# Kernel tuning notes

Measured on AMD Instinct MI355X. Metric: run time of the kernel, lower is better.

Reference implementation:

```python
import jax, jax.numpy as jnp
import numpy as np

FACTOR = 2  # upsample factor per spatial dim


def setup_inputs() -> dict:
    key = jax.random.key(0)
    k1, k2, k3 = jax.random.split(key, 3)
    B, C_in, C_out, H, W_ = 8, 128, 128, 64, 64
    x = jax.random.normal(k1, (B, C_in, H, W_), dtype=jnp.float32)
    # conv3x3 params (OIHW), fan-in scaled init like torch Conv2d default scale
    fan_in = C_in * 3 * 3
    W = jax.random.normal(k2, (C_out, C_in, 3, 3), dtype=jnp.float32) / np.sqrt(fan_in)
    b = jax.random.normal(k3, (C_out,), dtype=jnp.float32) * 0.01
    return {"x": x, "W": W, "b": b}


def reference(x, W, b):
    h = jnp.repeat(jnp.repeat(x, FACTOR, axis=2), FACTOR, axis=3)  # [B,C,2H,2W]
    # conv3x3: stride 1, padding 1
    out = jax.lax.conv_general_dilated(
        h, W,
        window_strides=(1, 1),
        padding=((1, 1), (1, 1)),
        dimension_numbers=("NCHW", "OIHW", "NCHW"),
    )
    return out + b[None, :, None, None]
```

## Files before the change

### kernel.cpp

```cpp
#include <hip/hip_runtime.h>
#include <stdint.h>

typedef short bf16x8 __attribute__((ext_vector_type(8)));
typedef float f32x4 __attribute__((ext_vector_type(4)));
typedef float f32x16 __attribute__((ext_vector_type(16)));

#define NCI 128
#define NCO 128
#define HIN 64
#define HP  66
#define NB  8

__device__ __forceinline__ unsigned short f32_to_bf16(float f) {
    union { float f; uint32_t u; } v; v.f = f;
    return (unsigned short)((v.u + 0x7FFFu + ((v.u >> 16) & 1u)) >> 16);
}

__device__ __forceinline__ void gl_lds16(const void* g, void* l) {
    __builtin_amdgcn_global_load_lds(
        (const __attribute__((address_space(1))) unsigned int*)g,
        (__attribute__((address_space(3))) unsigned int*)l, 16, 0, 0);
}

__device__ __forceinline__ float weff_sum(const float* wp, int py, int px, int ty, int tx) {
    float s = 0.f;
    #pragma unroll
    for (int ky = 0; ky < 3; ++ky) {
        bool iy = (py == 0) ? (ty == 0 ? (ky == 0) : (ky >= 1))
                            : (ty == 0 ? (ky <= 1) : (ky == 2));
        if (!iy) continue;
        #pragma unroll
        for (int kx = 0; kx < 3; ++kx) {
            bool ix = (px == 0) ? (tx == 0 ? (kx == 0) : (kx >= 1))
                                : (tx == 0 ? (kx <= 1) : (kx == 2));
            if (ix) s += wp[ky * 3 + kx];
        }
    }
    return s;
}

__global__ __launch_bounds__(256) void prep_kernel(
        const float* __restrict__ W, const float* __restrict__ x,
        unsigned short* __restrict__ Aw8, unsigned short* __restrict__ xq) {
    if (blockIdx.x < 1024) {
        int idx = blockIdx.x * 256 + threadIdx.x;
        int e   = idx & 7;
        int l   = (idx >> 3) & 63;
        int fm  = (idx >> 9) & 1;
        int s   = (idx >> 10) & 31;
        int coh = (idx >> 15) & 1;
        int par = idx >> 16;
        int co = coh * 64 + fm * 32 + (l & 31);
        int k  = s * 16 + (l >> 5) * 8 + e;
        int tap = k >> 7, ci = k & 127;
        Aw8[idx] = f32_to_bf16(weff_sum(W + (co * NCI + ci) * 9,
                                        par >> 1, par & 1, tap >> 1, tap & 1));
    } else {
        const int bb = blockIdx.x - 1024;
        const int b = bb / HP, hp = bb % HP;
        const int t = threadIdx.x;
        if (hp == 0 || hp == HP - 1) {
            bf16x8 z = (bf16x8){0, 0, 0, 0, 0, 0, 0, 0};
            for (int i = t; i < 4 * HP * 4; i += 256) {
                int g = i / (HP * 4), rem = i % (HP * 4);
                unsigned short* dst = xq +
                    ((((size_t)(b * 4 + g) * HP + hp) * HP) << 5) + rem * 8;
                *(bf16x8*)dst = z;
            }
            return;
        }
        const int h = hp - 1;
        if (t < 32) {
            bf16x8 z = (bf16x8){0, 0, 0, 0, 0, 0, 0, 0};
            int g = t >> 3, wpc = ((t >> 2) & 1) * (HP - 1), q = t & 3;
            unsigned short* dst = xq +
                ((((size_t)(b * 4 + g) * HP + hp) * HP + wpc) << 5) + q * 8;
            *(bf16x8*)dst = z;
        }
        const int w = t & 63, g = t >> 6;
        const float* src = x + ((size_t)(b * NCI + g * 32) * (HIN * HIN)) + h * HIN + w;
        unsigned short* dst = xq +
            ((((size_t)(b * 4 + g) * HP + hp) * HP + (w + 1)) << 5);
        #pragma unroll
        for (int q = 0; q < 4; ++q) {
            bf16x8 v;
            #pragma unroll
            for (int j = 0; j < 8; ++j)
                v[j] = (short)f32_to_bf16(src[(size_t)(q * 8 + j) * (HIN * HIN)]);
            *(bf16x8*)(dst + q * 8) = v;
        }
    }
}

__global__ __launch_bounds__(512, 2) void upconv16_kernel(
        const unsigned short* __restrict__ xq, const unsigned short* __restrict__ Aw8,
        const float* __restrict__ bv, float* __restrict__ out) {
    __shared__ __align__(16) unsigned short A_lds[32768];
    __shared__ __align__(16) unsigned short B_lds[42240];
    const int d = blockIdx.x;
    const int bi  = d & 7;
    const int py  = (d >> 3) & 1;
    const int px  = (d >> 4) & 1;
    const int coh = (d >> 5) & 1;
    const int ys  = d >> 6;
    const int tid = threadIdx.x, lane = tid & 63, wv = tid >> 6;
    const int sph = wv & 1, ol = wv >> 1;
    const int l31 = lane & 31, lh = lane >> 5;
    const int par = py * 2 + px;

    const unsigned short* Ag = Aw8 + (((size_t)(par * 2 + coh)) << 15);
    #pragma unroll
    for (int i = 0; i < 8; ++i) {
        const int u = i * 512 + tid;
        gl_lds16(Ag + u * 8, &A_lds[u * 8]);
    }
    #pragma unroll
    for (int i = 0; i < 11; ++i) {
        const int u = i * 512 + tid;
        if (u < 5280) {
            const int qs = u & 15, cell = u >> 4;
            const int r = cell / 66, c = cell - r * 66;
            const int q = qs ^ (c & 15);
            const int hp = ys * 4 + py + r;
            const unsigned short* gb = xq +
                ((((size_t)(bi * 4 + (q >> 2)) * HP + hp) * HP + c) << 5) + (q & 3) * 8;
            gl_lds16(gb, &B_lds[u * 8]);
        }
    }
    asm volatile("s_waitcnt vmcnt(0)" ::: "memory");
    __builtin_amdgcn_s_barrier();

    f32x16 acc[2];
    #pragma unroll
    for (int i = 0; i < 2; ++i)
        #pragma unroll
        for (int q = 0; q < 16; ++q)
            acc[i][q] = 0.f;

    #pragma unroll
    for (int s = 0; s < 32; ++s) {
        const int ty = s >> 4, tx = (s >> 3) & 1;
        const int q = (s & 7) * 2 + lh;
        const int r = ol + ty;
        const int c = sph * 32 + l31 + px + tx;
        const int qs = q ^ (c & 15);
        const bf16x8 bfr = *(const bf16x8*)&B_lds[(((r * 66 + c) << 4) + qs) * 8];
        const unsigned short* ap = &A_lds[(s << 10) + lane * 8];
        __builtin_amdgcn_s_setprio(1);
        acc[0] = __builtin_amdgcn_mfma_f32_32x32x16_bf16(
            *(const bf16x8*)ap, bfr, acc[0], 0, 0, 0);
        acc[1] = __builtin_amdgcn_mfma_f32_32x32x16_bf16(
            *(const bf16x8*)(ap + 512), bfr, acc[1], 0, 0, 0);
        __builtin_amdgcn_s_setprio(0);
    }

    const int yy = 2 * (ys * 4 + ol) + py;
    const int xx = 2 * (sph * 32 + l31) + px;
    #pragma unroll
    for (int fm = 0; fm < 2; ++fm) {
        #pragma unroll
        for (int j = 0; j < 16; ++j) {
            const int row = (j & 3) + 8 * (j >> 2) + 4 * lh;
            const int co = coh * 64 + fm * 32 + row;
            out[(((size_t)(bi * NCO + co)) << 14) + yy * 128 + xx] = acc[fm][j] + bv[co];
        }
    }
}

__global__ void weff_flat_kernel(const float* __restrict__ W,
                                 unsigned short* __restrict__ Aw) {
    int idx = blockIdx.x * 256 + threadIdx.x;
    int par = idx >> 16;
    int co  = (idx >> 9) & 127;
    int k   = idx & 511;
    int tap = k >> 7, ci = k & 127;
    Aw[idx] = f32_to_bf16(weff_sum(W + (co * NCI + ci) * 9,
                                   par >> 1, par & 1, tap >> 1, tap & 1));
}

__global__ __launch_bounds__(256) void upconv_fb_kernel(
        const float* __restrict__ x, const unsigned short* __restrict__ Aw,
        const float* __restrict__ bv, float* __restrict__ out) {
    __shared__ __align__(16) unsigned short A_lds[128 * 32];
    __shared__ __align__(16) unsigned short B_lds[128 * 32];
    const int par = blockIdx.y, py = par >> 1, px = par & 1;
    const int s0 = blockIdx.x * 128;
    const int bimg = s0 >> 12;
    const int oy0 = (s0 >> 6) & 63;
    const int tid = threadIdx.x;
    const int lane = tid & 63, wave = tid >> 6;
    const int wm = wave >> 1, wn = wave & 1;
    const float* xb = x + bimg * (NCI * HIN * HIN);
    f32x4 acc[4][4];
    #pragma unroll
    for (int i = 0; i < 4; ++i)
        #pragma unroll
        for (int j = 0; j < 4; ++j)
            acc[i][j] = (f32x4){0.f, 0.f, 0.f, 0.f};
    for (int kt = 0; kt < 16; ++kt) {
        const int tap = kt >> 2, ci0 = (kt & 3) * 32;
        const int ty = tap >> 1, tx = tap & 1;
        #pragma unroll
        for (int i = 0; i < 2; ++i) {
            int c = i * 256 + tid;
            *(bf16x8*)(&A_lds[c * 8]) = *(const bf16x8*)(Aw +
                ((par * 128 + (c >> 2)) * 512 + kt * 32 + (c & 3) * 8));
        }
        #pragma unroll
        for (int i = 0; i < 2; ++i) {
            int tsk = i * 256 + tid;
            int n = tsk & 127, kg = tsk >> 7;
            int r = n >> 6, ox = n & 63;
            int row = oy0 + r - 1 + py + ty;
            int col = ox - 1 + px + tx;
            bool ok = (row >= 0) & (row < HIN) & (col >= 0) & (col < HIN);
            const float* xp = xb + (((ci0 + kg * 8) * HIN + row) * HIN + col);
            bf16x8 v;
            #pragma unroll
            for (int q = 0; q < 8; ++q) {
                float f = ok ? xp[q * (HIN * HIN)] : 0.f;
                v[q] = (short)f32_to_bf16(f);
            }
            *(bf16x8*)(&B_lds[n * 32 + kg * 8]) = v;
        }
        __syncthreads();
        const int seg = (lane >> 4) * 8, rl2 = lane & 15;
        bf16x8 af[4], bfr[4];
        #pragma unroll
        for (int f = 0; f < 4; ++f)
            af[f] = *(const bf16x8*)(&A_lds[(wm * 64 + f * 16 + rl2) * 32 + seg]);
        #pragma unroll
        for (int f = 0; f < 4; ++f)
            bfr[f] = *(const bf16x8*)(&B_lds[(wn * 64 + f * 16 + rl2) * 32 + seg]);
        #pragma unroll
        for (int fm = 0; fm < 4; ++fm)
            #pragma unroll
            for (int fn = 0; fn < 4; ++fn)
                acc[fm][fn] = __builtin_amdgcn_mfma_f32_16x16x32_bf16(
                    af[fm], bfr[fn], acc[fm][fn], 0, 0, 0);
        __syncthreads();
    }
    #pragma unroll
    for (int fm = 0; fm < 4; ++fm) {
        const int co_b = wm * 64 + fm * 16 + (lane >> 4) * 4;
        float bias4[4];
        #pragma unroll
        for (int j = 0; j < 4; ++j) bias4[j] = bv[co_b + j];
        #pragma unroll
        for (int fn = 0; fn < 4; ++fn) {
            int n = wn * 64 + fn * 16 + (lane & 15);
            int s = s0 + n;
            int ox = s & 63, oy = (s >> 6) & 63, bi2 = s >> 12;
            int yy = 2 * oy + py, xx = 2 * ox + px;
            float* op = out + ((size_t)bi2 * 128 * 128 * 128) + (size_t)yy * 128 + xx;
            #pragma unroll
            for (int j = 0; j < 4; ++j)
                op[(size_t)(co_b + j) * (128 * 128)] = acc[fm][fn][j] + bias4[j];
        }
    }
}

extern "C" void kernel_launch(void* const* d_in, const int* in_sizes, int n_in,
                              void* d_out, int out_size, void* d_ws, size_t ws_size,
                              hipStream_t stream) {
    const float* x  = (const float*)d_in[0];
    const float* W  = (const float*)d_in[1];
    const float* bv = (const float*)d_in[2];
    float* out = (float*)d_out;
    unsigned short* Aw = (unsigned short*)d_ws;
    const size_t aw_bytes = (size_t)4 * 2 * 32 * 2 * 512 * sizeof(unsigned short);
    const size_t xq_bytes = (size_t)NB * 4 * HP * HP * 32 * sizeof(unsigned short);

    if (ws_size >= aw_bytes + xq_bytes) {
        unsigned short* xq = (unsigned short*)((char*)d_ws + aw_bytes);
        prep_kernel<<<1024 + NB * HP, 256, 0, stream>>>(W, x, Aw, xq);
        upconv16_kernel<<<1024, 512, 0, stream>>>(xq, Aw, bv, out);
    } else {
        weff_flat_kernel<<<1024, 256, 0, stream>>>(W, Aw);
        upconv_fb_kernel<<<dim3(256, 4), 256, 0, stream>>>(x, Aw, bv, out);
    }
}
```

Measured before the change: 41.40 us.

## Stream weights from global into registers, drop column padding, widen per-wave tile

The conv kernel now uses 256 threads, and each wave computes a 64x64 output tile (2x2 MFMA fragments) in place of a 64x32 one. Weight fragments are no longer staged in LDS; they are read straight from global memory into a triple-buffered register ring, prefetched three steps ahead. The padded-column layout of the quantized input is removed, and out-of-range columns are zeroed by a per-lane select, which shrinks LDS use and the prep work. This lowers LDS footprint and improves B-fragment reuse, at the cost of more registers, global-latency exposure on the weight loads, and extra select logic.

```diff
diff --git a/kernel.cpp b/kernel.cpp
--- a/kernel.cpp
+++ b/kernel.cpp
@@ -8,7 +8,6 @@
 #define NCI 128
 #define NCO 128
 #define HIN 64
-#define HP  66
 #define NB  8
 
 __device__ __forceinline__ unsigned short f32_to_bf16(float f) {
@@ -41,7 +40,7 @@
 
 __global__ __launch_bounds__(256) void prep_kernel(
         const float* __restrict__ W, const float* __restrict__ x,
-        unsigned short* __restrict__ Aw8, unsigned short* __restrict__ xq) {
+        unsigned short* __restrict__ Aw9, unsigned short* __restrict__ xq) {
     if (blockIdx.x < 1024) {
         int idx = blockIdx.x * 256 + threadIdx.x;
         int e   = idx & 7;
@@ -53,34 +52,26 @@
         int co = coh * 64 + fm * 32 + (l & 31);
         int k  = s * 16 + (l >> 5) * 8 + e;
         int tap = k >> 7, ci = k & 127;
-        Aw8[idx] = f32_to_bf16(weff_sum(W + (co * NCI + ci) * 9,
+        Aw9[idx] = f32_to_bf16(weff_sum(W + (co * NCI + ci) * 9,
                                         par >> 1, par & 1, tap >> 1, tap & 1));
     } else {
         const int bb = blockIdx.x - 1024;
-        const int b = bb / HP, hp = bb % HP;
+        const int b = bb / 66, hp = bb % 66;
         const int t = threadIdx.x;
-        if (hp == 0 || hp == HP - 1) {
+        unsigned short* rowp = xq + ((((size_t)b * 4) * 66 + hp) * 64) * 32;
+        if (hp == 0 || hp == 65) {
             bf16x8 z = (bf16x8){0, 0, 0, 0, 0, 0, 0, 0};
-            for (int i = t; i < 4 * HP * 4; i += 256) {
-                int g = i / (HP * 4), rem = i % (HP * 4);
-                unsigned short* dst = xq +
-                    ((((size_t)(b * 4 + g) * HP + hp) * HP) << 5) + rem * 8;
-                *(bf16x8*)dst = z;
+            for (int i = t; i < 1024; i += 256) {
+                int g = i >> 8, rem = i & 255;
+                int w = rem >> 2, q = rem & 3;
+                *(bf16x8*)(xq + (((((size_t)(b * 4 + g)) * 66 + hp) * 64 + w) << 5) + q * 8) = z;
             }
             return;
         }
         const int h = hp - 1;
-        if (t < 32) {
-            bf16x8 z = (bf16x8){0, 0, 0, 0, 0, 0, 0, 0};
-            int g = t >> 3, wpc = ((t >> 2) & 1) * (HP - 1), q = t & 3;
-            unsigned short* dst = xq +
-                ((((size_t)(b * 4 + g) * HP + hp) * HP + wpc) << 5) + q * 8;
-            *(bf16x8*)dst = z;
-        }
         const int w = t & 63, g = t >> 6;
         const float* src = x + ((size_t)(b * NCI + g * 32) * (HIN * HIN)) + h * HIN + w;
-        unsigned short* dst = xq +
-            ((((size_t)(b * 4 + g) * HP + hp) * HP + (w + 1)) << 5);
+        unsigned short* dst = xq + (((((size_t)(b * 4 + g)) * 66 + hp) * 64 + w) << 5);
         #pragma unroll
         for (int q = 0; q < 4; ++q) {
             bf16x8 v;
@@ -92,77 +83,91 @@
     }
 }
 
-__global__ __launch_bounds__(512, 2) void upconv16_kernel(
-        const unsigned short* __restrict__ xq, const unsigned short* __restrict__ Aw8,
+__global__ __launch_bounds__(256, 2) void upconv17_kernel(
+        const unsigned short* __restrict__ xq, const unsigned short* __restrict__ Aw9,
         const float* __restrict__ bv, float* __restrict__ out) {
-    __shared__ __align__(16) unsigned short A_lds[32768];
-    __shared__ __align__(16) unsigned short B_lds[42240];
+    __shared__ __align__(16) unsigned short B_lds[40960];
     const int d = blockIdx.x;
     const int bi  = d & 7;
     const int py  = (d >> 3) & 1;
     const int px  = (d >> 4) & 1;
     const int coh = (d >> 5) & 1;
     const int ys  = d >> 6;
-    const int tid = threadIdx.x, lane = tid & 63, wv = tid >> 6;
-    const int sph = wv & 1, ol = wv >> 1;
+    const int tid = threadIdx.x, lane = tid & 63, ol = tid >> 6;
     const int l31 = lane & 31, lh = lane >> 5;
     const int par = py * 2 + px;
 
-    const unsigned short* Ag = Aw8 + (((size_t)(par * 2 + coh)) << 15);
-    #pragma unroll
-    for (int i = 0; i < 8; ++i) {
-        const int u = i * 512 + tid;
-        gl_lds16(Ag + u * 8, &A_lds[u * 8]);
-    }
-    #pragma unroll
-    for (int i = 0; i < 11; ++i) {
-        const int u = i * 512 + tid;
-        if (u < 5280) {
-            const int qs = u & 15, cell = u >> 4;
-            const int r = cell / 66, c = cell - r * 66;
-            const int q = qs ^ (c & 15);
-            const int hp = ys * 4 + py + r;
-            const unsigned short* gb = xq +
-                ((((size_t)(bi * 4 + (q >> 2)) * HP + hp) * HP + c) << 5) + (q & 3) * 8;
-            gl_lds16(gb, &B_lds[u * 8]);
-        }
-    }
+    #pragma unroll
+    for (int i = 0; i < 20; ++i) {
+        const int u = i * 256 + tid;
+        const int qs = u & 15, cell = u >> 4;
+        const int r = cell >> 6, w = cell & 63;
+        const int q = qs ^ (w & 15);
+        const int hp = ys * 4 + py + r;
+        const unsigned short* gb = xq +
+            (((((size_t)(bi * 4 + (q >> 2))) * 66 + hp) * 64 + w) << 5) + (q & 3) * 8;
+        gl_lds16(gb, &B_lds[u * 8]);
+    }
+
+    const unsigned short* Ag = Aw9 + (((size_t)(par * 2 + coh)) << 15);
+    bf16x8 Abuf[3][2];
+    auto loadA = [&](bf16x8* Ad, int s) {
+        const unsigned short* p = Ag + (s << 10) + lane * 8;
+        Ad[0] = *(const bf16x8*)p;
+        Ad[1] = *(const bf16x8*)(p + 512);
+    };
+    loadA(Abuf[0], 0);
+    loadA(Abuf[1], 1);
+    loadA(Abuf[2], 2);
     asm volatile("s_waitcnt vmcnt(0)" ::: "memory");
     __builtin_amdgcn_s_barrier();
 
-    f32x16 acc[2];
+    f32x16 acc[2][2];
     #pragma unroll
     for (int i = 0; i < 2; ++i)
         #pragma unroll
-        for (int q = 0; q < 16; ++q)
-            acc[i][q] = 0.f;
+        for (int j = 0; j < 2; ++j)
+            #pragma unroll
+            for (int q = 0; q < 16; ++q)
+                acc[i][j][q] = 0.f;
 
     #pragma unroll
     for (int s = 0; s < 32; ++s) {
+        bf16x8* Ac = Abuf[s % 3];
         const int ty = s >> 4, tx = (s >> 3) & 1;
         const int q = (s & 7) * 2 + lh;
         const int r = ol + ty;
-        const int c = sph * 32 + l31 + px + tx;
-        const int qs = q ^ (c & 15);
-        const bf16x8 bfr = *(const bf16x8*)&B_lds[(((r * 66 + c) << 4) + qs) * 8];
-        const unsigned short* ap = &A_lds[(s << 10) + lane * 8];
         __builtin_amdgcn_s_setprio(1);
-        acc[0] = __builtin_amdgcn_mfma_f32_32x32x16_bf16(
-            *(const bf16x8*)ap, bfr, acc[0], 0, 0, 0);
-        acc[1] = __builtin_amdgcn_mfma_f32_32x32x16_bf16(
-            *(const bf16x8*)(ap + 512), bfr, acc[1], 0, 0, 0);
+        #pragma unroll
+        for (int fn = 0; fn < 2; ++fn) {
+            const int wr = fn * 32 + l31 + px + tx - 1;
+            const bool valid = (unsigned)wr < 64u;
+            const int w = valid ? wr : 0;
+            const int qs = q ^ (w & 15);
+            bf16x8 bfr = *(const bf16x8*)&B_lds[(((r << 6) + w) * 16 + qs) * 8];
+            bfr = valid ? bfr : (bf16x8){0, 0, 0, 0, 0, 0, 0, 0};
+            #pragma unroll
+            for (int fm = 0; fm < 2; ++fm)
+                acc[fm][fn] = __builtin_amdgcn_mfma_f32_32x32x16_bf16(
+                    Ac[fm], bfr, acc[fm][fn], 0, 0, 0);
+        }
         __builtin_amdgcn_s_setprio(0);
+        if (s + 3 < 32) loadA(Abuf[s % 3], s + 3);
     }
 
     const int yy = 2 * (ys * 4 + ol) + py;
-    const int xx = 2 * (sph * 32 + l31) + px;
     #pragma unroll
     for (int fm = 0; fm < 2; ++fm) {
         #pragma unroll
-        for (int j = 0; j < 16; ++j) {
-            const int row = (j & 3) + 8 * (j >> 2) + 4 * lh;
-            const int co = coh * 64 + fm * 32 + row;
-            out[(((size_t)(bi * NCO + co)) << 14) + yy * 128 + xx] = acc[fm][j] + bv[co];
+        for (int fn = 0; fn < 2; ++fn) {
+            const int xx = 2 * (fn * 32 + l31) + px;
+            #pragma unroll
+            for (int j = 0; j < 16; ++j) {
+                const int row = (j & 3) + 8 * (j >> 2) + 4 * lh;
+                const int co = coh * 64 + fm * 32 + row;
+                out[(((size_t)(bi * NCO + co)) << 14) + yy * 128 + xx] =
+                    acc[fm][fn][j] + bv[co];
+            }
         }
     }
 }
@@ -269,12 +274,12 @@
     float* out = (float*)d_out;
     unsigned short* Aw = (unsigned short*)d_ws;
     const size_t aw_bytes = (size_t)4 * 2 * 32 * 2 * 512 * sizeof(unsigned short);
-    const size_t xq_bytes = (size_t)NB * 4 * HP * HP * 32 * sizeof(unsigned short);
+    const size_t xq_bytes = (size_t)NB * 4 * 66 * 64 * 32 * sizeof(unsigned short);
 
     if (ws_size >= aw_bytes + xq_bytes) {
         unsigned short* xq = (unsigned short*)((char*)d_ws + aw_bytes);
-        prep_kernel<<<1024 + NB * HP, 256, 0, stream>>>(W, x, Aw, xq);
-        upconv16_kernel<<<1024, 512, 0, stream>>>(xq, Aw, bv, out);
+        prep_kernel<<<1024 + 528, 256, 0, stream>>>(W, x, Aw, xq);
+        upconv17_kernel<<<1024, 256, 0, stream>>>(xq, Aw, bv, out);
     } else {
         weff_flat_kernel<<<1024, 256, 0, stream>>>(W, Aw);
         upconv_fb_kernel<<<dim3(256, 4), 256, 0, stream>>>(x, Aw, bv, out);
```

After: 41.24 us. No clear change (-0.4%).
